# Kernel tuning notes

Measured on AMD Instinct MI355X. Metric: run time of the kernel, lower is better.

Reference implementation:

```python
import jax, jax.numpy as jnp
import numpy as np

N_TYPES = 2
N_NODES = 50000
N_EDGES = 400000
C = 128
H = 4
D = C // H
L = 2
# edge type e connects src node type META[e][0] -> dst node type META[e][1]
META = ((0, 1), (1, 0))


def setup_inputs() -> dict:
    key = jax.random.key(0)
    ks = jax.random.split(key, 16)
    s = 0.05
    return {
        "x": jax.random.normal(ks[0], (N_TYPES, N_NODES, C), jnp.float32),
        "edge_index": jax.random.randint(ks[1], (2, 2, N_EDGES), 0, N_NODES, jnp.int64),
        "Wk": jax.random.normal(ks[2], (L, N_TYPES, C, C), jnp.float32) * s,
        "bk": jax.random.normal(ks[3], (L, N_TYPES, C), jnp.float32) * s,
        "Wq": jax.random.normal(ks[4], (L, N_TYPES, C, C), jnp.float32) * s,
        "bq": jax.random.normal(ks[5], (L, N_TYPES, C), jnp.float32) * s,
        "Wv": jax.random.normal(ks[6], (L, N_TYPES, C, C), jnp.float32) * s,
        "bv": jax.random.normal(ks[7], (L, N_TYPES, C), jnp.float32) * s,
        "Wa": jax.random.normal(ks[8], (L, N_TYPES, C, C), jnp.float32) * s,
        "ba": jax.random.normal(ks[9], (L, N_TYPES, C), jnp.float32) * s,
        "skip": jax.random.normal(ks[10], (L, N_TYPES), jnp.float32),
        "a_rel": jax.random.normal(ks[11], (L, 2, H, D, D), jnp.float32) * s,
        "m_rel": jax.random.normal(ks[12], (L, 2, H, D, D), jnp.float32) * s,
        "p_rel": jnp.ones((L, 2, H), jnp.float32),
        "ln_g": jnp.ones((L, N_TYPES, C), jnp.float32),
        "ln_b": jnp.zeros((L, N_TYPES, C), jnp.float32),
    }


def _layer(x, edge_index, Wk, bk, Wq, bq, Wv, bv, Wa, ba, skip, a_rel, m_rel, p_rel, ln_g, ln_b):
    # x: [T, N, C] ; per-type K/Q/V projections -> [T, N, H, D]
    k = (jnp.einsum('tnc,tcd->tnd', x, Wk) + bk[:, None]).reshape(N_TYPES, N_NODES, H, D)
    q = (jnp.einsum('tnc,tcd->tnd', x, Wq) + bq[:, None]).reshape(N_TYPES, N_NODES, H, D)
    v = (jnp.einsum('tnc,tcd->tnd', x, Wv) + bv[:, None]).reshape(N_TYPES, N_NODES, H, D)
    scale = 1.0 / float(np.sqrt(D))
    out = jnp.zeros((N_TYPES, N_NODES, H, D), x.dtype)
    for e, (st, dt) in enumerate(META):
        si, di = edge_index[e, 0], edge_index[e, 1]
        # per-relation transforms of gathered src keys/values: [E, H, D]
        k_rel = jnp.einsum('ehd,hdf->ehf', k[st][si], a_rel[e])
        v_rel = jnp.einsum('ehd,hdf->ehf', v[st][si], m_rel[e])
        # attention logits [E, H], softmax grouped by destination node
        att = jnp.sum(q[dt][di] * k_rel, axis=-1) * p_rel[e] * scale
        amax = jax.ops.segment_max(att, di, num_segments=N_NODES)
        att = jnp.exp(att - amax[di])
        den = jax.ops.segment_sum(att, di, num_segments=N_NODES)
        att = att / (den[di] + 1e-16)
        agg = jax.ops.segment_sum(att[..., None] * v_rel, di, num_segments=N_NODES)
        out = out.at[dt].add(agg)
    o = out.reshape(N_TYPES, N_NODES, C)
    o = jnp.einsum('tnc,tcd->tnd', jax.nn.gelu(o), Wa) + ba[:, None]
    beta = jax.nn.sigmoid(skip)[:, None, None]
    x = beta * o + (1.0 - beta) * x
    # per-type LayerNorm over features, then ReLU
    mu = jnp.mean(x, axis=-1, keepdims=True)
    var = jnp.var(x, axis=-1, keepdims=True)
    x = (x - mu) * jax.lax.rsqrt(var + 1e-5) * ln_g[:, None] + ln_b[:, None]
    return jax.nn.relu(x)


def reference(x, edge_index, Wk, bk, Wq, bq, Wv, bv, Wa, ba, skip, a_rel, m_rel, p_rel, ln_g, ln_b):
    for l in range(L):
        x = _layer(x, edge_index, Wk[l], bk[l], Wq[l], bq[l], Wv[l], bv[l],
                   Wa[l], ba[l], skip[l], a_rel[l], m_rel[l], p_rel[l], ln_g[l], ln_b[l])
    # x_dict[entity_table]: return node type 0 ("user") embeddings
    return x[0]
```

## Files before the change

### kernel.cpp

```cpp
#include <hip/hip_runtime.h>

#define NN 50000
#define EE 400000
#define CC 128
#define TT 2
#define NT16R 3128

typedef float floatx4 __attribute__((ext_vector_type(4)));
typedef float floatx2 __attribute__((ext_vector_type(2)));
typedef _Float16 half8 __attribute__((ext_vector_type(8)));
typedef _Float16 half2t __attribute__((ext_vector_type(2)));

__device__ __forceinline__ unsigned pk2h(float a, float b) {
    return __builtin_bit_cast(unsigned, __builtin_amdgcn_cvt_pkrtz(a, b));
}
__device__ __forceinline__ float gelu_f(float x) {
    float u = 0.7978845608028654f * (x + 0.044715f * x * x * x);
    float t = __expf(2.f * u);
    return x * (1.f - 1.f / (t + 1.f));
}

__device__ __forceinline__ floatx2 pkfma(floatx2 a, floatx2 b, floatx2 c) {
#if __has_builtin(__builtin_elementwise_fma)
    return __builtin_elementwise_fma(a, b, c);
#else
    floatx2 r;
    r.x = fmaf(a.x, b.x, c.x);
    r.y = fmaf(a.y, b.y, c.y);
    return r;
#endif
}

__device__ __forceinline__ unsigned pk_fp8x4(float a, float b, float c, float d) {
#if __has_builtin(__builtin_amdgcn_cvt_pk_fp8_f32)
    int v = 0;
    v = __builtin_amdgcn_cvt_pk_fp8_f32(a, b, v, false);
    v = __builtin_amdgcn_cvt_pk_fp8_f32(c, d, v, true);
    return (unsigned)v;
#else
    auto enc = [](float x) -> unsigned {
        unsigned u = __float_as_uint(x);
        unsigned s = (u >> 24) & 0x80;
        int e = (int)((u >> 23) & 0xff);
        unsigned m = u & 0x7fffff;
        if (e == 0) return s;
        int ne = e - 127 + 7;
        if (ne <= 0) {
            unsigned full = (1u << 23) | m;
            int sh = 21 - ne;
            if (sh > 24) return s;
            unsigned r = full >> sh;
            unsigned rem = full & ((1u << sh) - 1);
            unsigned half = 1u << (sh - 1);
            if (rem > half || (rem == half && (r & 1))) r++;
            return s | (r & 0x7f);
        }
        unsigned r = m >> 20;
        unsigned rem = m & 0xfffff;
        if (rem > 0x80000 || (rem == 0x80000 && (r & 1))) {
            r++;
            if (r == 8) { r = 0; ne++; }
        }
        if (ne > 15) return s | 0x7e;
        return s | ((unsigned)ne << 3) | r;
    };
    return enc(a) | (enc(b) << 8) | (enc(c) << 16) | (enc(d) << 24);
#endif
}

template <bool HI>
__device__ __forceinline__ floatx2 upk_fp8(unsigned v) {
#if __has_builtin(__builtin_amdgcn_cvt_pk_f32_fp8)
    return __builtin_amdgcn_cvt_pk_f32_fp8((int)v, HI);
#else
    auto dec = [](unsigned b) -> float {
        unsigned s = b & 0x80;
        unsigned e = (b >> 3) & 0xf;
        unsigned m = b & 7;
        float val;
        if (e == 0) val = (float)m * (1.f / 512.f);
        else val = (1.f + (float)m * 0.125f) * exp2f((float)e - 7.f);
        return s ? -val : val;
    };
    unsigned base = HI ? (v >> 16) : v;
    floatx2 r;
    r.x = dec(base & 0xff);
    r.y = dec((base >> 8) & 0xff);
    return r;
#endif
}

__global__ void k_detect(const int* __restrict__ ei, int* __restrict__ flag) {
    if (threadIdx.x == 0 && blockIdx.x == 0) {
        int orv = 0;
        for (int i = 1; i < 64; i += 2) orv |= ei[i];
        flag[0] = (orv == 0) ? 1 : 0;
    }
}

__global__ void k_count(const int* __restrict__ ei, const int* __restrict__ flag,
                        int* __restrict__ counts) {
    int i = blockIdx.x * 256 + threadIdx.x;
    if (i >= 2 * EE) return;
    int is64 = flag[0];
    int e = i / EE, j = i - e * EE;
    size_t pos = (size_t)(e * 2 + 1) * EE + j;
    int di = is64 ? ei[pos * 2] : ei[pos];
    di = min(max(di, 0), NN - 1);
    atomicAdd(&counts[e * NN + di], 1);
}

#define SCB ((NN + 1023) / 1024)
__global__ __launch_bounds__(256) void k_scan1(const int* __restrict__ counts,
                                               int* __restrict__ rowptr,
                                               int* __restrict__ bsum) {
    int e = blockIdx.y, b = blockIdx.x;
    int tid = threadIdx.x, lane = tid & 63, wid = tid >> 6;
    __shared__ int wsum[4];
    int base = b * 1024 + tid * 4;
    int v[4], s = 0;
#pragma unroll
    for (int k2 = 0; k2 < 4; k2++) {
        int i = base + k2;
        v[k2] = (i < NN) ? counts[e * NN + i] : 0;
        s += v[k2];
    }
    int incl = s;
#pragma unroll
    for (int off = 1; off < 64; off <<= 1) {
        int t2 = __shfl_up(incl, off);
        if (lane >= off) incl += t2;
    }
    if (lane == 63) wsum[wid] = incl;
    __syncthreads();
    int woff = 0;
    for (int w2 = 0; w2 < wid; w2++) woff += wsum[w2];
    int excl = woff + incl - s;
#pragma unroll
    for (int k2 = 0; k2 < 4; k2++) {
        int i = base + k2;
        if (i < NN) rowptr[e * (NN + 1) + i] = excl;
        excl += v[k2];
    }
    if (tid == 255) bsum[e * SCB + b] = woff + incl;
}

__global__ void k_scan2(int* __restrict__ bsum, int* __restrict__ rowptr) {
    int e = threadIdx.x >> 6, lane = threadIdx.x & 63;
    int v = (lane < SCB) ? bsum[e * SCB + lane] : 0;
    int incl = v;
#pragma unroll
    for (int off = 1; off < 64; off <<= 1) {
        int t2 = __shfl_up(incl, off);
        if (lane >= off) incl += t2;
    }
    if (lane < SCB) bsum[e * SCB + lane] = incl - v;
    if (lane == 63) rowptr[e * (NN + 1) + NN] = incl;
}

__global__ __launch_bounds__(256) void k_scan3(int* __restrict__ rowptr,
                                               const int* __restrict__ bsum,
                                               int* __restrict__ cursor) {
    int e = blockIdx.y, b = blockIdx.x;
    int off = bsum[e * SCB + b];
    int base = b * 1024 + threadIdx.x * 4;
#pragma unroll
    for (int k2 = 0; k2 < 4; k2++) {
        int i = base + k2;
        if (i < NN) {
            int r = rowptr[e * (NN + 1) + i] + off;
            rowptr[e * (NN + 1) + i] = r;
            cursor[e * NN + i] = r;
        }
    }
}

__global__ void k_scatter(const int* __restrict__ ei, const int* __restrict__ flag,
                          int* __restrict__ cursor, int* __restrict__ csr) {
    int i = blockIdx.x * 256 + threadIdx.x;
    if (i >= 2 * EE) return;
    int is64 = flag[0];
    int e = i / EE, j = i - e * EE;
    size_t ps = (size_t)(e * 2 + 0) * EE + j;
    size_t pd = (size_t)(e * 2 + 1) * EE + j;
    int si = is64 ? ei[ps * 2] : ei[ps];
    int di = is64 ? ei[pd * 2] : ei[pd];
    si = min(max(si, 0), NN - 1);
    di = min(max(di, 0), NN - 1);
    int pos = atomicAdd(&cursor[e * NN + di], 1);
    csr[(size_t)e * EE + pos] = si;
}

__global__ __launch_bounds__(256) void k_cvt(const float* __restrict__ x,
                                             _Float16* __restrict__ xs) {
    __shared__ _Float16 sm[64 * 132];
    int t = blockIdx.y;
    int tid = threadIdx.x;
    int node0 = blockIdx.x * 64;
#pragma unroll
    for (int p = 0; p < 8; p++) {
        int c = p * 256 + tid;
        int row = c >> 5, ch = c & 31;
        int node = min(node0 + row, NN - 1);
        float4 v = *(const float4*)(x + ((size_t)t * NN + node) * CC + ch * 4);
        uint2 o;
        o.x = pk2h(v.x, v.y);
        o.y = pk2h(v.z, v.w);
        *(uint2*)(sm + row * 132 + ch * 4) = o;
    }
    __syncthreads();
    _Float16* xt = xs + (size_t)t * NT16R * 2048;
#pragma unroll
    for (int p = 0; p < 4; p++) {
        int c = p * 256 + tid;
        int tl = c >> 8, kt = (c >> 6) & 3, l = c & 63;
        int q = l >> 4, ln = l & 15;
        *(uint4*)(xt + ((size_t)(blockIdx.x * 4 + tl) * 4 + kt) * 512 + l * 8) =
            *(const uint4*)(sm + (tl * 16 + ln) * 132 + kt * 32 + q * 8);
    }
}

__global__ void k_prep(const float* __restrict__ Wk, const float* __restrict__ Wq,
                       const float* __restrict__ Wv, const float* __restrict__ Wa,
                       const float* __restrict__ bk, const float* __restrict__ bq,
                       const float* __restrict__ bv,
                       const float* __restrict__ a_rel, const float* __restrict__ m_rel,
                       const float* __restrict__ p_rel,
                       _Float16* __restrict__ W2, _Float16* __restrict__ Wa2,
                       float* __restrict__ beff) {
    const float SCALE = 0.17677669529663687f;
    int l = blockIdx.y;
    int idx = blockIdx.x * 256 + threadIdx.x;
    if (idx < 2 * 384 * 128) {
        int t = idx / (384 * 128);
        int r = idx - t * 384 * 128;
        int n = r >> 7, k = r & 127;
        float val;
        if (n < 128) {
            val = Wq[((l * 2 + t) * 128 + k) * 128 + n] *
                  p_rel[(l * 2 + (1 - t)) * 4 + (n >> 5)] * SCALE;
        } else if (n < 256) {
            int nn = n - 128, h = nn >> 5, f = nn & 31;
            const float* wr = Wk + ((l * 2 + t) * 128 + k) * 128 + h * 32;
            const float* ar = a_rel + (((l * 2 + t) * 4 + h) * 32) * 32 + f;
            float s = 0.f;
            for (int d = 0; d < 32; d++) s += wr[d] * ar[d * 32];
            val = s;
        } else {
            int nn = n - 256, h = nn >> 5, f = nn & 31;
            const float* wr = Wv + ((l * 2 + t) * 128 + k) * 128 + h * 32;
            const float* mr = m_rel + (((l * 2 + t) * 4 + h) * 32) * 32 + f;
            float s = 0.f;
            for (int d = 0; d < 32; d++) s += wr[d] * mr[d * 32];
            val = s;
        }
        W2[(((size_t)(l * 2 + t) * 24 + (n >> 4)) * 4 + (k >> 5)) * 512 +
           (((k & 31) >> 3) * 16 + (n & 15)) * 8 + (k & 7)] = (_Float16)val;
    } else if (idx < 2 * 384 * 128 + 2 * 128 * 128) {
        int r = idx - 2 * 384 * 128;
        int t = r / (128 * 128);
        r -= t * 128 * 128;
        int n = r >> 7, k = r & 127;
        float val = Wa[((l * 2 + t) * 128 + k) * 128 + n];
        Wa2[(((size_t)(l * 2 + t) * 8 + (n >> 4)) * 4 + (k >> 5)) * 512 +
            (((k & 31) >> 3) * 16 + (n & 15)) * 8 + (k & 7)] = (_Float16)val;
    } else if (idx < 2 * 384 * 128 + 2 * 128 * 128 + 2 * 384) {
        int r = idx - (2 * 384 * 128 + 2 * 128 * 128);
        int t = r / 384, n = r - t * 384;
        float val;
        if (n < 128) {
            val = bq[(l * 2 + t) * 128 + n] * p_rel[(l * 2 + (1 - t)) * 4 + (n >> 5)] * SCALE;
        } else if (n < 256) {
            int nn = n - 128, h = nn >> 5, f = nn & 31;
            float s = 0.f;
            for (int d = 0; d < 32; d++)
                s += bk[(l * 2 + t) * 128 + h * 32 + d] *
                     a_rel[(((l * 2 + t) * 4 + h) * 32 + d) * 32 + f];
            val = s;
        } else {
            int nn = n - 256, h = nn >> 5, f = nn & 31;
            float s = 0.f;
            for (int d = 0; d < 32; d++)
                s += bv[(l * 2 + t) * 128 + h * 32 + d] *
                     m_rel[(((l * 2 + t) * 4 + h) * 32 + d) * 32 + f];
            val = s;
        }
        beff[(l * 2 + t) * 384 + n] = val;
    }
}

template <int NT, int COL0>
__global__ __launch_bounds__(256) void k_gemm_qkv(const _Float16* __restrict__ xs,
                                                  const _Float16* __restrict__ W2,
                                                  const float* __restrict__ beff,
                                                  unsigned char* __restrict__ qkv8, int l,
                                                  int t0) {
    constexpr int RB = (NT == 6) ? 512 : 256;
    constexpr int RS = RB + 16;
    __shared__ unsigned char tile[32 * RS];
    int t = t0 + blockIdx.y;
    int tid = threadIdx.x;
    int wid = tid >> 6, lane = tid & 63;
    int quad = lane >> 4, ln = lane & 15;
    int node0 = blockIdx.x * 32;
    int tile0 = blockIdx.x * 2;
    int lt = l * 2 + t;
    const _Float16* Wt = W2 + (size_t)lt * 24 * 2048;
    const _Float16* xt = xs + (size_t)t * NT16R * 2048;
    half8 bf[2][4];
#pragma unroll
    for (int ns = 0; ns < 2; ns++)
#pragma unroll
        for (int kt = 0; kt < 4; kt++)
            bf[ns][kt] = *(const half8*)(xt + ((size_t)(tile0 + ns) * 4 + kt) * 512 + lane * 8);
    floatx4 acc[NT][2];
#pragma unroll
    for (int nt = 0; nt < NT; nt++)
#pragma unroll
        for (int ns = 0; ns < 2; ns++) acc[nt][ns] = (floatx4){0.f, 0.f, 0.f, 0.f};
#pragma unroll
    for (int nt = 0; nt < NT; nt++) {
        int mt = COL0 / 16 + wid * NT + nt;
#pragma unroll
        for (int kt = 0; kt < 4; kt++) {
            half8 af = *(const half8*)(Wt + ((size_t)mt * 4 + kt) * 512 + lane * 8);
            acc[nt][0] = __builtin_amdgcn_mfma_f32_16x16x32_f16(af, bf[0][kt], acc[nt][0], 0, 0, 0);
            acc[nt][1] = __builtin_amdgcn_mfma_f32_16x16x32_f16(af, bf[1][kt], acc[nt][1], 0, 0, 0);
        }
    }
#pragma unroll
    for (int nt = 0; nt < NT; nt++) {
        int c0 = COL0 + wid * NT * 16 + nt * 16 + quad * 4;
        float4 b4 = *(const float4*)(beff + (l * 2 + t) * 384 + c0);
#pragma unroll
        for (int ns = 0; ns < 2; ns++) {
            int nl = ns * 16 + ln;
            float v0 = acc[nt][ns][0] + b4.x, v1 = acc[nt][ns][1] + b4.y;
            float v2 = acc[nt][ns][2] + b4.z, v3 = acc[nt][ns][3] + b4.w;
            unsigned char* rowp = tile + nl * RS;
            if (c0 < 128) {
                uint2 o;
                o.x = pk2h(v0, v1);
                o.y = pk2h(v2, v3);
                *(uint2*)(rowp + 2 * c0) = o;
            } else {
                int f0 = c0 & 127;
                int isV = (c0 >= 256);
                int loff = (f0 >> 3) * 16 + (f0 & 7) + isV * 8 +
                           ((COL0 == 128) ? 0 : 256);
                *(unsigned*)(rowp + loff) = pk_fp8x4(v0, v1, v2, v3);
            }
        }
    }
    __syncthreads();
    constexpr int CPR = RB / 16;
    constexpr int PASSES = (32 * CPR) / 256;
#pragma unroll
    for (int p = 0; p < PASSES; p++) {
        int c = p * 256 + tid;
        int row = c / CPR, ch = c - row * CPR;
        int node = node0 + row;
        if (node < NN)
            *(uint4*)(qkv8 + ((size_t)t * NN + node) * 512 + (COL0 ? 256 : 0) + ch * 16) =
                *(const uint4*)(tile + row * RS + ch * 16);
    }
}

__global__ __launch_bounds__(256) void k_attn(const unsigned char* __restrict__ qkv8,
                                              const int* __restrict__ rowptr,
                                              const int* __restrict__ csr,
                                              _Float16* __restrict__ outg) {
    int t = blockIdx.y;
    int e = 1 - t;
    int st = 1 - t;
    int wid = threadIdx.x >> 6, lane = threadIdx.x & 63;
    int n = __builtin_amdgcn_readfirstlane(blockIdx.x * 4 + wid);
    int e4 = lane >> 4, s = lane & 15;
    int r0 = rowptr[e * (NN + 1) + n];
    int r1 = rowptr[e * (NN + 1) + n + 1];
    const int* csrp = csr + (size_t)e * EE;
    const unsigned char* sbase = qkv8 + (size_t)st * NN * 512;
    uint4 qd = *(const uint4*)(qkv8 + ((size_t)t * NN + n) * 512 + s * 16);

    floatx2 acc2[4];
#pragma unroll
    for (int i = 0; i < 4; i++) acc2[i] = (floatx2){0.f, 0.f};
    float lsum = 0.f;
    floatx2 q2[4];

    auto process = [&](const uint4& u, float msk) {
        floatx2 p2 = q2[0] * upk_fp8<false>(u.x);
        p2 = pkfma(q2[1], upk_fp8<true>(u.x), p2);
        p2 = pkfma(q2[2], upk_fp8<false>(u.y), p2);
        p2 = pkfma(q2[3], upk_fp8<true>(u.y), p2);
        float p = p2.x + p2.y;
        p += __shfl_xor(p, 1);
        p += __shfl_xor(p, 2);
        float w = __expf(p) * msk;
        lsum += w;
        floatx2 w2 = (floatx2){w, w};
        acc2[0] = pkfma(w2, upk_fp8<false>(u.z), acc2[0]);
        acc2[1] = pkfma(w2, upk_fp8<true>(u.z), acc2[1]);
        acc2[2] = pkfma(w2, upk_fp8<false>(u.w), acc2[2]);
        acc2[3] = pkfma(w2, upk_fp8<true>(u.w), acc2[3]);
    };

    if (r0 < r1) {
        int j = r0;
        int iA = csrp[min(j + e4, r1 - 1)];
        int iB = csrp[min(j + 4 + e4, r1 - 1)];
        uint4 uA = (uint4){0u, 0u, 0u, 0u};
        if (j + e4 < r1) uA = *(const uint4*)(sbase + (size_t)iA * 512 + 256 + s * 16);
        {
            half2t h0 = __builtin_bit_cast(half2t, qd.x), h1 = __builtin_bit_cast(half2t, qd.y);
            half2t h2 = __builtin_bit_cast(half2t, qd.z), h3 = __builtin_bit_cast(half2t, qd.w);
            q2[0] = (floatx2){(float)h0.x, (float)h0.y};
            q2[1] = (floatx2){(float)h1.x, (float)h1.y};
            q2[2] = (floatx2){(float)h2.x, (float)h2.y};
            q2[3] = (floatx2){(float)h3.x, (float)h3.y};
        }
        for (; j + 8 < r1; j += 4) {
            uint4 uB = *(const uint4*)(sbase + (size_t)iB * 512 + 256 + s * 16);
            iB = csrp[min(j + 8 + e4, r1 - 1)];
            process(uA, 1.f);
            uA = uB;
        }
        if (j + 4 < r1) {
            uint4 uB = (uint4){0u, 0u, 0u, 0u};
            float mB = (j + 4 + e4 < r1) ? 1.f : 0.f;
            if (j + 4 + e4 < r1)
                uB = *(const uint4*)(sbase + (size_t)iB * 512 + 256 + s * 16);
            process(uA, 1.f);
            process(uB, mB);
        } else {
            process(uA, (j + e4 < r1) ? 1.f : 0.f);
        }
    }
    float accf[8] = {acc2[0].x, acc2[0].y, acc2[1].x, acc2[1].y,
                     acc2[2].x, acc2[2].y, acc2[3].x, acc2[3].y};
#pragma unroll
    for (int i = 0; i < 8; i++) {
        accf[i] += __shfl_xor(accf[i], 16);
        accf[i] += __shfl_xor(accf[i], 32);
    }
    lsum += __shfl_xor(lsum, 16);
    lsum += __shfl_xor(lsum, 32);
    float inv = 1.f / (lsum + 1e-16f);
    if (e4 == 0) {
        uint4 o;
        o.x = pk2h(accf[0] * inv, accf[1] * inv);
        o.y = pk2h(accf[2] * inv, accf[3] * inv);
        o.z = pk2h(accf[4] * inv, accf[5] * inv);
        o.w = pk2h(accf[6] * inv, accf[7] * inv);
        *(uint4*)(outg + ((size_t)t * NN + n) * CC + s * 8) = o;
    }
}

__global__ __launch_bounds__(256) void k_epilogue(
    const _Float16* __restrict__ outg, const _Float16* __restrict__ Wa2,
    const float* __restrict__ ba, const float* __restrict__ skipv,
    const float* __restrict__ ln_g, const float* __restrict__ ln_b,
    const _Float16* __restrict__ xs_cur, _Float16* __restrict__ xs_next,
    float* __restrict__ xout, int l) {
    __shared__ float smem[64 * 130];
    _Float16* smem_h = (_Float16*)smem;
    int t = blockIdx.y;
    int tid = threadIdx.x;
    int wid = tid >> 6, lane = tid & 63;
    int quad = lane >> 4, ln = lane & 15;
    int node0 = blockIdx.x * 64;
    int nloc = wid * 16 + ln;
    int node = node0 + nloc;
    int arow = min(node, NN - 1);
    const _Float16* grow = outg + ((size_t)t * NN + arow) * CC;
    half8 bf[4];
#pragma unroll
    for (int kt = 0; kt < 4; kt++) {
        uint4 gd = *(const uint4*)(grow + kt * 32 + quad * 8);
        half2t h0 = __builtin_bit_cast(half2t, gd.x), h1 = __builtin_bit_cast(half2t, gd.y);
        half2t h2 = __builtin_bit_cast(half2t, gd.z), h3 = __builtin_bit_cast(half2t, gd.w);
        uint4 pk;
        pk.x = pk2h(gelu_f((float)h0.x), gelu_f((float)h0.y));
        pk.y = pk2h(gelu_f((float)h1.x), gelu_f((float)h1.y));
        pk.z = pk2h(gelu_f((float)h2.x), gelu_f((float)h2.y));
        pk.w = pk2h(gelu_f((float)h3.x), gelu_f((float)h3.y));
        bf[kt] = __builtin_bit_cast(half8, pk);
    }
    const _Float16* Wt = Wa2 + (size_t)(l * 2 + t) * 8 * 2048;
    floatx4 acc[8];
#pragma unroll
    for (int nt = 0; nt < 8; nt++) acc[nt] = (floatx4){0.f, 0.f, 0.f, 0.f};
#pragma unroll
    for (int nt = 0; nt < 8; nt++) {
#pragma unroll
        for (int kt = 0; kt < 4; kt++) {
            half8 af = *(const half8*)(Wt + ((size_t)nt * 4 + kt) * 512 + lane * 8);
            acc[nt] = __builtin_amdgcn_mfma_f32_16x16x32_f16(af, bf[kt], acc[nt], 0, 0, 0);
        }
    }
    float sv = skipv[l * TT + t];
    float beta = 1.f / (1.f + __expf(-sv));
    const _Float16* xt = xs_cur + (size_t)t * NT16R * 2048;
    int tileR = arow >> 4, lnR = arow & 15;
    float xn[8][4];
    float s1 = 0.f, s2 = 0.f;
#pragma unroll
    for (int nt = 0; nt < 8; nt++) {
        int c0 = nt * 16 + quad * 4;
        float4 b4 = *(const float4*)(ba + (l * TT + t) * CC + c0);
        uint2 xw = *(const uint2*)(xt + ((size_t)tileR * 4 + (c0 >> 5)) * 512 +
                                   (((c0 >> 3) & 3) * 16 + lnR) * 8 + (c0 & 7));
        half2t x0 = __builtin_bit_cast(half2t, xw.x), x1 = __builtin_bit_cast(half2t, xw.y);
        float xv[4] = {(float)x0.x, (float)x0.y, (float)x1.x, (float)x1.y};
        float bb[4] = {b4.x, b4.y, b4.z, b4.w};
#pragma unroll
        for (int reg = 0; reg < 4; reg++) {
            float o = acc[nt][reg] + bb[reg];
            float v = beta * o + (1.f - beta) * xv[reg];
            xn[nt][reg] = v;
            s1 += v;
            s2 += v * v;
        }
    }
    s1 += __shfl_xor(s1, 16); s1 += __shfl_xor(s1, 32);
    s2 += __shfl_xor(s2, 16); s2 += __shfl_xor(s2, 32);
    float mu = s1 * (1.f / CC);
    float var = s2 * (1.f / CC) - mu * mu;
    float rs = rsqrtf(var + 1e-5f);
#pragma unroll
    for (int nt = 0; nt < 8; nt++) {
        int c0 = nt * 16 + quad * 4;
        float4 g4 = *(const float4*)(ln_g + (l * TT + t) * CC + c0);
        float4 be4 = *(const float4*)(ln_b + (l * TT + t) * CC + c0);
        float y0 = fmaxf((xn[nt][0] - mu) * rs * g4.x + be4.x, 0.f);
        float y1 = fmaxf((xn[nt][1] - mu) * rs * g4.y + be4.y, 0.f);
        float y2 = fmaxf((xn[nt][2] - mu) * rs * g4.z + be4.z, 0.f);
        float y3 = fmaxf((xn[nt][3] - mu) * rs * g4.w + be4.w, 0.f);
        if (xout) {
            float4 o4 = {y0, y1, y2, y3};
            *(float4*)(smem + nloc * 130 + c0) = o4;
        } else {
            uint2 o;
            o.x = pk2h(y0, y1);
            o.y = pk2h(y2, y3);
            *(uint2*)(smem_h + nloc * 132 + c0) = o;
        }
    }
    __syncthreads();
    if (xout) {
#pragma unroll
        for (int p = 0; p < 8; p++) {
            int c = p * 256 + tid;
            int row = c >> 5, ch = c & 31;
            int nd = node0 + row;
            if (nd < NN)
                *(uint4*)(xout + (size_t)nd * CC + ch * 4) =
                    *(const uint4*)(smem + row * 130 + ch * 4);
        }
    } else {
        _Float16* xnt = xs_next + (size_t)t * NT16R * 2048;
#pragma unroll
        for (int p = 0; p < 4; p++) {
            int c = p * 256 + tid;
            int tl = c >> 8, kt2 = (c >> 6) & 3, l2 = c & 63;
            int q2 = l2 >> 4, ln2 = l2 & 15;
            *(uint4*)(xnt + ((size_t)(blockIdx.x * 4 + tl) * 4 + kt2) * 512 + l2 * 8) =
                *(const uint4*)(smem_h + (tl * 16 + ln2) * 132 + kt2 * 32 + q2 * 8);
        }
    }
}

extern "C" void kernel_launch(void* const* d_in, const int* in_sizes, int n_in,
                              void* d_out, int out_size, void* d_ws, size_t ws_size,
                              hipStream_t stream) {
    const float* x = (const float*)d_in[0];
    const int* ei = (const int*)d_in[1];
    const float* Wk = (const float*)d_in[2];
    const float* bk = (const float*)d_in[3];
    const float* Wq = (const float*)d_in[4];
    const float* bq = (const float*)d_in[5];
    const float* Wv = (const float*)d_in[6];
    const float* bv = (const float*)d_in[7];
    const float* Wa = (const float*)d_in[8];
    const float* ba = (const float*)d_in[9];
    const float* skip = (const float*)d_in[10];
    const float* a_rel = (const float*)d_in[11];
    const float* m_rel = (const float*)d_in[12];
    const float* p_rel = (const float*)d_in[13];
    const float* ln_g = (const float*)d_in[14];
    const float* ln_b = (const float*)d_in[15];

    char* ws = (char*)d_ws;
    size_t off = 0;
    auto alloc = [&](size_t b) {
        size_t o = off;
        off = (off + b + 255) & ~(size_t)255;
        return o;
    };
    _Float16* xsA = (_Float16*)(ws + alloc((size_t)TT * NT16R * 2048 * 2));
    _Float16* xsB = (_Float16*)(ws + alloc((size_t)TT * NT16R * 2048 * 2));
    unsigned char* qkv8 = (unsigned char*)(ws + alloc((size_t)TT * NN * 512));
    _Float16* outg = (_Float16*)(ws + alloc((size_t)TT * NN * CC * 2));
    _Float16* W2 = (_Float16*)(ws + alloc((size_t)2 * TT * 24 * 2048 * 2));
    _Float16* Wa2 = (_Float16*)(ws + alloc((size_t)2 * TT * 8 * 2048 * 2));
    float* beff = (float*)(ws + alloc((size_t)2 * TT * 384 * 4));
    int* counts = (int*)(ws + alloc((size_t)2 * NN * 4));
    int* cursor = (int*)(ws + alloc((size_t)2 * NN * 4));
    int* rowptr = (int*)(ws + alloc((size_t)2 * (NN + 1) * 4));
    int* csr = (int*)(ws + alloc((size_t)2 * EE * 4));
    int* flag = (int*)(ws + alloc(256));
    int* bsum = (int*)(ws + alloc((size_t)2 * SCB * 4 + 256));
    (void)ws_size; (void)in_sizes; (void)n_in; (void)out_size;

    k_detect<<<1, 64, 0, stream>>>(ei, flag);
    (void)hipMemsetAsync(counts, 0, (size_t)2 * NN * 4, stream);
    k_count<<<(2 * EE + 255) / 256, 256, 0, stream>>>(ei, flag, counts);
    k_scan1<<<dim3(SCB, 2), 256, 0, stream>>>(counts, rowptr, bsum);
    k_scan2<<<1, 128, 0, stream>>>(bsum, rowptr);
    k_scan3<<<dim3(SCB, 2), 256, 0, stream>>>(rowptr, bsum, cursor);
    k_scatter<<<(2 * EE + 255) / 256, 256, 0, stream>>>(ei, flag, cursor, csr);
    k_cvt<<<dim3(NT16R / 4, 2), 256, 0, stream>>>(x, xsA);
    k_prep<<<dim3((2 * 384 * 128 + 2 * 128 * 128 + 2 * 384 + 255) / 256, 2), 256, 0, stream>>>(
        Wk, Wq, Wv, Wa, bk, bq, bv, a_rel, m_rel, p_rel, W2, Wa2, beff);

    const int GB = (NN + 31) / 32;
    k_gemm_qkv<6, 0><<<dim3(GB, 2), 256, 0, stream>>>(xsA, W2, beff, qkv8, 0, 0);
    k_attn<<<dim3(NN / 4, 2), 256, 0, stream>>>(qkv8, rowptr, csr, outg);
    k_epilogue<<<dim3((NN + 63) / 64, 2), 256, 0, stream>>>(
        outg, Wa2, ba, skip, ln_g, ln_b, xsA, xsB, nullptr, 0);
    k_gemm_qkv<2, 0><<<dim3(GB, 1), 256, 0, stream>>>(xsB, W2, beff, qkv8, 1, 0);
    k_gemm_qkv<4, 128><<<dim3(GB, 1), 256, 0, stream>>>(xsB, W2, beff, qkv8, 1, 1);
    k_attn<<<dim3(NN / 4, 1), 256, 0, stream>>>(qkv8, rowptr, csr, outg);
    k_epilogue<<<dim3((NN + 63) / 64, 1), 256, 0, stream>>>(
        outg, Wa2, ba, skip, ln_g, ln_b, xsB, nullptr, (float*)d_out, 1);
}
```

Baseline: 380.5 us.

## Record per-edge rank during counting to drop scatter-phase atomics

The counting kernel now keeps the value returned by each atomicAdd as a per-edge rank and stores it as a 16-bit value. The scatter kernel then computes each edge's CSR position as rowptr plus rank, with no second atomic pass and no cursor array. Both kernels also handle 8 edges per thread so several loads and atomics are in flight at once. This adds a 2-byte-per-edge rank buffer that must be written and read back, and it assumes no node's in-degree reaches 65536.

New measurement: 349.0 us. 1.09x faster.

```diff
diff --git a/kernel.cpp b/kernel.cpp
--- a/kernel.cpp
+++ b/kernel.cpp
@@ -5,6 +5,7 @@
 #define CC 128
 #define TT 2
 #define NT16R 3128
+#define KPB 8
 
 typedef float floatx4 __attribute__((ext_vector_type(4)));
 typedef float floatx2 __attribute__((ext_vector_type(2)));
@@ -98,16 +99,34 @@
     }
 }
 
-__global__ void k_count(const int* __restrict__ ei, const int* __restrict__ flag,
-                        int* __restrict__ counts) {
-    int i = blockIdx.x * 256 + threadIdx.x;
-    if (i >= 2 * EE) return;
+__global__ __launch_bounds__(256) void k_count(const int* __restrict__ ei,
+                                               const int* __restrict__ flag,
+                                               int* __restrict__ counts,
+                                               unsigned short* __restrict__ rank) {
+    int e = blockIdx.y;
+    int tid = threadIdx.x;
+    int base = blockIdx.x * (256 * KPB);
     int is64 = flag[0];
-    int e = i / EE, j = i - e * EE;
-    size_t pos = (size_t)(e * 2 + 1) * EE + j;
-    int di = is64 ? ei[pos * 2] : ei[pos];
-    di = min(max(di, 0), NN - 1);
-    atomicAdd(&counts[e * NN + di], 1);
+    const size_t db = (size_t)(e * 2 + 1) * EE;
+    int di[KPB];
+    bool val[KPB];
+#pragma unroll
+    for (int k = 0; k < KPB; k++) {
+        int j = base + k * 256 + tid;
+        val[k] = j < EE;
+        int jc = val[k] ? j : 0;
+        int d = is64 ? ei[(db + jc) * 2] : ei[db + jc];
+        di[k] = min(max(d, 0), NN - 1);
+    }
+    int rk[KPB];
+#pragma unroll
+    for (int k = 0; k < KPB; k++)
+        rk[k] = val[k] ? atomicAdd(&counts[e * NN + di[k]], 1) : 0;
+#pragma unroll
+    for (int k = 0; k < KPB; k++) {
+        int j = base + k * 256 + tid;
+        if (val[k]) rank[(size_t)e * EE + j] = (unsigned short)rk[k];
+    }
 }
 
 #define SCB ((NN + 1023) / 1024)
@@ -159,36 +178,50 @@
 }
 
 __global__ __launch_bounds__(256) void k_scan3(int* __restrict__ rowptr,
-                                               const int* __restrict__ bsum,
-                                               int* __restrict__ cursor) {
+                                               const int* __restrict__ bsum) {
     int e = blockIdx.y, b = blockIdx.x;
     int off = bsum[e * SCB + b];
     int base = b * 1024 + threadIdx.x * 4;
 #pragma unroll
     for (int k2 = 0; k2 < 4; k2++) {
         int i = base + k2;
-        if (i < NN) {
-            int r = rowptr[e * (NN + 1) + i] + off;
-            rowptr[e * (NN + 1) + i] = r;
-            cursor[e * NN + i] = r;
-        }
-    }
-}
-
-__global__ void k_scatter(const int* __restrict__ ei, const int* __restrict__ flag,
-                          int* __restrict__ cursor, int* __restrict__ csr) {
-    int i = blockIdx.x * 256 + threadIdx.x;
-    if (i >= 2 * EE) return;
+        if (i < NN) rowptr[e * (NN + 1) + i] += off;
+    }
+}
+
+__global__ __launch_bounds__(256) void k_scatter(const int* __restrict__ ei,
+                                                 const int* __restrict__ flag,
+                                                 const int* __restrict__ rowptr,
+                                                 const unsigned short* __restrict__ rank,
+                                                 int* __restrict__ csr) {
+    int e = blockIdx.y;
+    int tid = threadIdx.x;
+    int base = blockIdx.x * (256 * KPB);
     int is64 = flag[0];
-    int e = i / EE, j = i - e * EE;
-    size_t ps = (size_t)(e * 2 + 0) * EE + j;
-    size_t pd = (size_t)(e * 2 + 1) * EE + j;
-    int si = is64 ? ei[ps * 2] : ei[ps];
-    int di = is64 ? ei[pd * 2] : ei[pd];
-    si = min(max(si, 0), NN - 1);
-    di = min(max(di, 0), NN - 1);
-    int pos = atomicAdd(&cursor[e * NN + di], 1);
-    csr[(size_t)e * EE + pos] = si;
+    const size_t sb = (size_t)(e * 2 + 0) * EE;
+    const size_t db = (size_t)(e * 2 + 1) * EE;
+    int si[KPB], di[KPB], rk[KPB];
+#pragma unroll
+    for (int k = 0; k < KPB; k++) {
+        int j = base + k * 256 + tid;
+        int jc = (j < EE) ? j : 0;
+        si[k] = is64 ? ei[(sb + jc) * 2] : ei[sb + jc];
+        di[k] = is64 ? ei[(db + jc) * 2] : ei[db + jc];
+        rk[k] = rank[(size_t)e * EE + jc];
+    }
+    int pos[KPB];
+#pragma unroll
+    for (int k = 0; k < KPB; k++) {
+        di[k] = min(max(di[k], 0), NN - 1);
+        si[k] = min(max(si[k], 0), NN - 1);
+    }
+#pragma unroll
+    for (int k = 0; k < KPB; k++) pos[k] = rowptr[e * (NN + 1) + di[k]] + rk[k];
+#pragma unroll
+    for (int k = 0; k < KPB; k++) {
+        int j = base + k * 256 + tid;
+        if (j < EE) csr[(size_t)e * EE + pos[k]] = si[k];
+    }
 }
 
 __global__ __launch_bounds__(256) void k_cvt(const float* __restrict__ x,
@@ -605,7 +638,7 @@
     _Float16* Wa2 = (_Float16*)(ws + alloc((size_t)2 * TT * 8 * 2048 * 2));
     float* beff = (float*)(ws + alloc((size_t)2 * TT * 384 * 4));
     int* counts = (int*)(ws + alloc((size_t)2 * NN * 4));
-    int* cursor = (int*)(ws + alloc((size_t)2 * NN * 4));
+    unsigned short* rankb = (unsigned short*)(ws + alloc((size_t)2 * EE * 2));
     int* rowptr = (int*)(ws + alloc((size_t)2 * (NN + 1) * 4));
     int* csr = (int*)(ws + alloc((size_t)2 * EE * 4));
     int* flag = (int*)(ws + alloc(256));
@@ -614,11 +647,12 @@
 
     k_detect<<<1, 64, 0, stream>>>(ei, flag);
     (void)hipMemsetAsync(counts, 0, (size_t)2 * NN * 4, stream);
-    k_count<<<(2 * EE + 255) / 256, 256, 0, stream>>>(ei, flag, counts);
+    const int EB = (EE + 256 * KPB - 1) / (256 * KPB);
+    k_count<<<dim3(EB, 2), 256, 0, stream>>>(ei, flag, counts, rankb);
     k_scan1<<<dim3(SCB, 2), 256, 0, stream>>>(counts, rowptr, bsum);
     k_scan2<<<1, 128, 0, stream>>>(bsum, rowptr);
-    k_scan3<<<dim3(SCB, 2), 256, 0, stream>>>(rowptr, bsum, cursor);
-    k_scatter<<<(2 * EE + 255) / 256, 256, 0, stream>>>(ei, flag, cursor, csr);
+    k_scan3<<<dim3(SCB, 2), 256, 0, stream>>>(rowptr, bsum);
+    k_scatter<<<dim3(EB, 2), 256, 0, stream>>>(ei, flag, rowptr, rankb, csr);
     k_cvt<<<dim3(NT16R / 4, 2), 256, 0, stream>>>(x, xsA);
     k_prep<<<dim3((2 * 384 * 128 + 2 * 128 * 128 + 2 * 384 + 255) / 256, 2), 256, 0, stream>>>(
         Wk, Wq, Wv, Wa, bk, bq, bv, a_rel, m_rel, p_rel, W2, Wa2, beff);
```
